# Kernel optimization log

Hardware: AMD Instinct MI355X
Metric: run time of the kernel (lower is better)

## Reference

```python
import jax, jax.numpy as jnp
import numpy as np

N_EMBED = 1024
N_HEAD = 16
HEAD_DIM = N_EMBED // N_HEAD
B, T = 64, 256
EPS = 1e-5


def _layernorm(x, w, b):
    mu = jnp.mean(x, axis=-1, keepdims=True)
    var = jnp.mean(jnp.square(x - mu), axis=-1, keepdims=True)
    return (x - mu) * jax.lax.rsqrt(var + EPS) * w + b


def setup_inputs() -> dict:
    key = jax.random.key(0)
    ks = jax.random.split(key, 8)
    s = lambda fan_in: 1.0 / np.sqrt(fan_in)
    return {
        "x": jax.random.normal(ks[0], (B, T, N_EMBED), dtype=jnp.float32),
        "ln1_w": jnp.ones((N_EMBED,), jnp.float32),
        "ln1_b": jnp.zeros((N_EMBED,), jnp.float32),
        # weights stored [in, out] (transposed vs torch Linear)
        "w_attn": jax.random.normal(ks[1], (N_EMBED, 3 * N_EMBED), jnp.float32) * s(N_EMBED),
        "b_attn": jnp.zeros((3 * N_EMBED,), jnp.float32),
        "w_proj": jax.random.normal(ks[2], (N_EMBED, N_EMBED), jnp.float32) * s(N_EMBED),
        "b_proj": jnp.zeros((N_EMBED,), jnp.float32),
        "ln2_w": jnp.ones((N_EMBED,), jnp.float32),
        "ln2_b": jnp.zeros((N_EMBED,), jnp.float32),
        "w_fc": jax.random.normal(ks[3], (N_EMBED, 4 * N_EMBED), jnp.float32) * s(N_EMBED),
        "b_fc": jnp.zeros((4 * N_EMBED,), jnp.float32),
        "w_out": jax.random.normal(ks[4], (4 * N_EMBED, N_EMBED), jnp.float32) * s(4 * N_EMBED),
        "b_out": jnp.zeros((N_EMBED,), jnp.float32),
    }


def reference(x, ln1_w, ln1_b, w_attn, b_attn, w_proj, b_proj,
              ln2_w, ln2_b, w_fc, b_fc, w_out, b_out):
    Bs, Ts, C = x.shape
    # --- attention branch (pre-norm) ---
    h = _layernorm(x, ln1_w, ln1_b)
    qkv = h @ w_attn + b_attn                      # [B,T,3C]
    q, k, v = jnp.split(qkv, 3, axis=-1)
    q = q.reshape(Bs, Ts, N_HEAD, HEAD_DIM).transpose(0, 2, 1, 3)  # [B,H,T,D]
    k = k.reshape(Bs, Ts, N_HEAD, HEAD_DIM).transpose(0, 2, 1, 3)
    v = v.reshape(Bs, Ts, N_HEAD, HEAD_DIM).transpose(0, 2, 1, 3)
    att = jnp.einsum("bhqd,bhkd->bhqk", q, k) * (1.0 / np.sqrt(HEAD_DIM))
    causal = jnp.tril(jnp.ones((Ts, Ts), dtype=bool))
    att = jnp.where(causal, att, -jnp.inf)
    att = jax.nn.softmax(att, axis=-1)
    y = jnp.einsum("bhqk,bhkd->bhqd", att, v)      # [B,H,T,D]
    y = y.transpose(0, 2, 1, 3).reshape(Bs, Ts, C)
    x = x + (y @ w_proj + b_proj)
    # --- MLP branch (pre-norm) ---
    h = _layernorm(x, ln2_w, ln2_b)
    h = jax.nn.gelu(h @ w_fc + b_fc, approximate=False)
    x = x + (h @ w_out + b_out)
    return x
```

## Files before the change

kernel.cpp:

```cpp
#include <hip/hip_runtime.h>
#include <math.h>


#define C_DIM   1024
#define NHEAD   16
#define HDIM    64
#define TSEQ    256
#define BATCH   64
#define KTILE   128

typedef __attribute__((ext_vector_type(4))) float fx4;
typedef __attribute__((ext_vector_type(8))) short sx8;

__device__ __forceinline__ ushort f2bf(float f) {
    uint x = __float_as_uint(f);
    x += 0x7fffu + ((x >> 16) & 1u);
    return (ushort)(x >> 16);
}
__device__ __forceinline__ float bf2f(ushort u) {
    return __uint_as_float(((uint)u) << 16);
}

__global__ __launch_bounds__(256)
void wconv(const float* __restrict__ W, ushort* __restrict__ Wt, int K, int N)
{
    __shared__ float T[64][65];
    const int kt = blockIdx.x << 6, nt = blockIdx.y << 6;
    const int ln = threadIdx.x & 63, g4 = threadIdx.x >> 6;
    #pragma unroll
    for (int i = 0; i < 16; ++i) {
        const int r = i * 4 + g4;
        T[r][ln] = W[(size_t)(kt + r) * N + nt + ln];
    }
    __syncthreads();
    #pragma unroll
    for (int i = 0; i < 16; ++i) {
        const int r = i * 4 + g4;
        Wt[(size_t)(nt + r) * K + kt + ln] = f2bf(T[ln][r]);
    }
}

__global__ __launch_bounds__(256)
void ln_bf16(const float* __restrict__ x, const float* __restrict__ w,
             const float* __restrict__ b, ushort* __restrict__ out)
{
    const int row = blockIdx.x;
    const int tid = threadIdx.x;
    const float4 v = reinterpret_cast<const float4*>(x + (size_t)row * C_DIM)[tid];

    float s  = v.x + v.y + v.z + v.w;
    float ss = v.x * v.x + v.y * v.y + v.z * v.z + v.w * v.w;
    #pragma unroll
    for (int off = 32; off > 0; off >>= 1) {
        s  += __shfl_down(s, off);
        ss += __shfl_down(ss, off);
    }
    __shared__ float rs[4], rss[4];
    const int wid = tid >> 6, lane = tid & 63;
    if (lane == 0) { rs[wid] = s; rss[wid] = ss; }
    __syncthreads();
    if (tid == 0) {
        const float S  = rs[0] + rs[1] + rs[2] + rs[3];
        const float SS = rss[0] + rss[1] + rss[2] + rss[3];
        const float mu  = S * (1.0f / C_DIM);
        const float var = SS * (1.0f / C_DIM) - mu * mu;
        rs[0]  = mu;
        rss[0] = rsqrtf(var + 1e-5f);
    }
    __syncthreads();
    const float mu = rs[0], rstd = rss[0];

    const float4 wv = reinterpret_cast<const float4*>(w)[tid];
    const float4 bv = reinterpret_cast<const float4*>(b)[tid];
    ushort4 o;
    o.x = f2bf((v.x - mu) * rstd * wv.x + bv.x);
    o.y = f2bf((v.y - mu) * rstd * wv.y + bv.y);
    o.z = f2bf((v.z - mu) * rstd * wv.z + bv.z);
    o.w = f2bf((v.w - mu) * rstd * wv.w + bv.w);
    reinterpret_cast<ushort4*>(out + (size_t)row * C_DIM)[tid] = o;
}

template<int EPI>
__global__ __launch_bounds__(256)
void gemm_mfma(const ushort* __restrict__ A, const ushort* __restrict__ Wt,
               const float* __restrict__ bias, const float* __restrict__ res,
               void* __restrict__ outv, int M, int N, int K)
{
    __shared__ ushort As[128 * 32];
    __shared__ ushort Bs[128 * 32];

    const int tid  = threadIdx.x;
    const int lane = tid & 63;
    const int wid  = tid >> 6;
    const int wr   = (wid >> 1) << 6;
    const int wc   = (wid & 1) << 6;
    const int bm = blockIdx.x << 7;
    const int bn = blockIdx.y << 7;

    const int srow = tid >> 2;
    const int spos = tid & 3;
    const int skg  = spos ^ ((srow >> 1) & 3);
    const size_t ga0 = (size_t)(bm + srow)      * K + skg * 8;
    const size_t ga1 = (size_t)(bm + srow + 64) * K + skg * 8;
    const size_t gb0 = (size_t)(bn + srow)      * K + skg * 8;
    const size_t gb1 = (size_t)(bn + srow + 64) * K + skg * 8;
    ushort* la0 = &As[srow * 32 + spos * 8];
    ushort* la1 = &As[(srow + 64) * 32 + spos * 8];
    ushort* lb0 = &Bs[srow * 32 + spos * 8];
    ushort* lb1 = &Bs[(srow + 64) * 32 + spos * 8];

    const int frow = lane & 15;
    const int fpos = ((lane >> 4) ^ ((frow >> 1) & 3)) * 8;
    int aoff[4], boff[4];
    #pragma unroll
    for (int i = 0; i < 4; ++i) {
        aoff[i] = (wr + i * 16 + frow) * 32 + fpos;
        boff[i] = (wc + i * 16 + frow) * 32 + fpos;
    }

    fx4 acc[4][4] = {};

    const int nk = K >> 5;
    sx8 ra0 = *(const sx8*)(A  + ga0);
    sx8 ra1 = *(const sx8*)(A  + ga1);
    sx8 rb0 = *(const sx8*)(Wt + gb0);
    sx8 rb1 = *(const sx8*)(Wt + gb1);

    for (int t = 0; t < nk; ++t) {
        __syncthreads();
        *(sx8*)la0 = ra0; *(sx8*)la1 = ra1;
        *(sx8*)lb0 = rb0; *(sx8*)lb1 = rb1;
        __syncthreads();
        if (t + 1 < nk) {
            const int ko = (t + 1) << 5;
            ra0 = *(const sx8*)(A  + ga0 + ko);
            ra1 = *(const sx8*)(A  + ga1 + ko);
            rb0 = *(const sx8*)(Wt + gb0 + ko);
            rb1 = *(const sx8*)(Wt + gb1 + ko);
        }
        sx8 af[4], bf[4];
        #pragma unroll
        for (int i = 0; i < 4; ++i) af[i] = *(const sx8*)&As[aoff[i]];
        #pragma unroll
        for (int i = 0; i < 4; ++i) bf[i] = *(const sx8*)&Bs[boff[i]];
        #pragma unroll
        for (int i = 0; i < 4; ++i)
            #pragma unroll
            for (int j = 0; j < 4; ++j)
                acc[i][j] = __builtin_amdgcn_mfma_f32_16x16x32_bf16(
                    af[i], bf[j], acc[i][j], 0, 0, 0);
    }

    const int r0 = bm + wr + (lane >> 4) * 4;
    const int c0 = bn + wc + (lane & 15);
    #pragma unroll
    for (int i = 0; i < 4; ++i) {
        #pragma unroll
        for (int r = 0; r < 4; ++r) {
            const int row = r0 + i * 16 + r;
            #pragma unroll
            for (int j = 0; j < 4; ++j) {
                const int col = c0 + j * 16;
                float v = acc[i][j][r] + bias[col];
                if (EPI == 1) {
                    v += res[(size_t)row * N + col];
                    ((float*)outv)[(size_t)row * N + col] = v;
                } else if (EPI == 2) {
                    v = 0.5f * v * (1.0f + erff(v * 0.70710678118654752f));
                    ((ushort*)outv)[(size_t)row * N + col] = f2bf(v);
                } else {
                    ((ushort*)outv)[(size_t)row * N + col] = f2bf(v);
                }
            }
        }
    }
}

__global__ __launch_bounds__(256)
void attn_kernel(const ushort* __restrict__ qkv, ushort* __restrict__ y)
{
    __shared__ float Ks[KTILE][HDIM];
    __shared__ float Vs[KTILE][HDIM];

    const int bl = blockIdx.x >> 4;
    const int h  = blockIdx.x & 15;
    const size_t base = (size_t)bl * TSEQ * 3072 + (size_t)h * HDIM;

    const int t = threadIdx.x;
    float q[HDIM];
    const ushort* qp = qkv + base + (size_t)t * 3072;
    #pragma unroll
    for (int i = 0; i < 8; ++i) {
        sx8 v8 = *(const sx8*)(qp + i * 8);
        #pragma unroll
        for (int j = 0; j < 8; ++j) q[i * 8 + j] = bf2f((ushort)v8[j]);
    }

    float acc[HDIM];
    #pragma unroll
    for (int d = 0; d < HDIM; ++d) acc[d] = 0.0f;
    float m = -INFINITY, l = 0.0f;
    const float scale = 0.125f;

    for (int ts = 0; ts < TSEQ; ts += KTILE) {
        __syncthreads();
        for (int idx = threadIdx.x; idx < KTILE * 8; idx += 256) {
            const int row = idx >> 3;
            const int c8  = (idx & 7) * 8;
            const ushort* p = qkv + base + (size_t)(ts + row) * 3072 + c8;
            sx8 kv = *(const sx8*)(p + 1024);
            sx8 vv = *(const sx8*)(p + 2048);
            #pragma unroll
            for (int j = 0; j < 8; ++j) {
                Ks[row][c8 + j] = bf2f((ushort)kv[j]);
                Vs[row][c8 + j] = bf2f((ushort)vv[j]);
            }
        }
        __syncthreads();

        const int ke = (t < ts + KTILE ? t : ts + KTILE - 1);
        for (int k = ts; k <= ke; ++k) {
            const int kr = k - ts;
            float s = 0.0f;
            #pragma unroll
            for (int d = 0; d < HDIM; ++d) s += q[d] * Ks[kr][d];
            s *= scale;
            const float mn = fmaxf(m, s);
            const float cold = __expf(m - mn);
            const float p    = __expf(s - mn);
            l = l * cold + p;
            #pragma unroll
            for (int d = 0; d < HDIM; ++d) acc[d] = acc[d] * cold + p * Vs[kr][d];
            m = mn;
        }
    }

    const float inv = 1.0f / l;
    ushort* yp = y + ((size_t)(bl * TSEQ + t)) * C_DIM + (size_t)h * HDIM;
    #pragma unroll
    for (int i = 0; i < 16; ++i) {
        ushort4 o;
        o.x = f2bf(acc[i * 4 + 0] * inv);
        o.y = f2bf(acc[i * 4 + 1] * inv);
        o.z = f2bf(acc[i * 4 + 2] * inv);
        o.w = f2bf(acc[i * 4 + 3] * inv);
        reinterpret_cast<ushort4*>(yp)[i] = o;
    }
}

extern "C" void kernel_launch(void* const* d_in, const int* in_sizes, int n_in,
                              void* d_out, int out_size, void* d_ws, size_t ws_size,
                              hipStream_t stream)
{
    const float* x      = (const float*)d_in[0];
    const float* ln1_w  = (const float*)d_in[1];
    const float* ln1_b  = (const float*)d_in[2];
    const float* w_attn = (const float*)d_in[3];
    const float* b_attn = (const float*)d_in[4];
    const float* w_proj = (const float*)d_in[5];
    const float* b_proj = (const float*)d_in[6];
    const float* ln2_w  = (const float*)d_in[7];
    const float* ln2_b  = (const float*)d_in[8];
    const float* w_fc   = (const float*)d_in[9];
    const float* b_fc   = (const float*)d_in[10];
    const float* w_out  = (const float*)d_in[11];
    const float* b_out  = (const float*)d_in[12];
    float* out = (float*)d_out;

    ushort* wbf     = (ushort*)d_ws;
    ushort* wt_attn = wbf;
    ushort* wt_proj = wbf + 3145728;
    ushort* wt_fc   = wbf + 4194304;
    ushort* wt_out  = wbf + 8388608;
    const size_t wbytes = 12582912ull * 2;

    int nchunk = 64;
    for (int cand = 1; cand <= 64; cand *= 2) {
        const size_t rows = (size_t)(BATCH / cand) * TSEQ;
        if (wbytes + rows * 10240ull <= ws_size) { nchunk = cand; break; }
    }
    const int bchunk = BATCH / nchunk;
    const int rows   = bchunk * TSEQ;

    ushort* hbuf = wbf + 12582912;
    ushort* qkvb = hbuf + (size_t)rows * 1024;
    ushort* ybuf = qkvb + (size_t)rows * 3072;
    ushort* act  = qkvb;

    wconv<<<dim3(16, 48), 256, 0, stream>>>(w_attn, wt_attn, 1024, 3072);
    wconv<<<dim3(16, 16), 256, 0, stream>>>(w_proj, wt_proj, 1024, 1024);
    wconv<<<dim3(16, 64), 256, 0, stream>>>(w_fc,   wt_fc,   1024, 4096);
    wconv<<<dim3(64, 16), 256, 0, stream>>>(w_out,  wt_out,  4096, 1024);

    for (int c = 0; c < nchunk; ++c) {
        const size_t r0 = (size_t)c * rows;
        const float* xc = x   + r0 * C_DIM;
        float*       oc = out + r0 * C_DIM;
        ln_bf16<<<rows, 256, 0, stream>>>(xc, ln1_w, ln1_b, hbuf);
        gemm_mfma<0><<<dim3(rows / 128, 3072 / 128), 256, 0, stream>>>(
            hbuf, wt_attn, b_attn, nullptr, qkvb, rows, 3072, 1024);
        attn_kernel<<<bchunk * NHEAD, 256, 0, stream>>>(qkvb, ybuf);
        gemm_mfma<1><<<dim3(rows / 128, 1024 / 128), 256, 0, stream>>>(
            ybuf, wt_proj, b_proj, xc, oc, rows, 1024, 1024);
    }

    for (int c = 0; c < nchunk; ++c) {
        const size_t r0 = (size_t)c * rows;
        float* oc = out + r0 * C_DIM;
        ln_bf16<<<rows, 256, 0, stream>>>(oc, ln2_w, ln2_b, hbuf);
        gemm_mfma<2><<<dim3(rows / 128, 4096 / 128), 256, 0, stream>>>(
            hbuf, wt_fc, b_fc, nullptr, act, rows, 4096, 1024);
        gemm_mfma<1><<<dim3(rows / 128, 1024 / 128), 256, 0, stream>>>(
            act, wt_out, b_out, oc, oc, rows, 1024, 4096);
    }
}
```

Measured before the change: 1.104 ms.

## Rewrite causal attention as MFMA flash-attention with bf16 LDS tiles

Replaces the scalar one-thread-per-query attention with a kernel where each wave handles 64 query rows. QK^T and PV use bf16 MFMA 16x16x32, and K plus transposed V are staged in LDS as bf16. Online softmax uses cross-lane shuffles, and probabilities are written to per-wave LDS before the PV multiply. Causal tiles above the diagonal are skipped. Load is unbalanced across waves, and P is rounded to bf16.

```diff
diff --git a/kernel.cpp b/kernel.cpp
--- a/kernel.cpp
+++ b/kernel.cpp
@@ -7,7 +7,6 @@
 #define HDIM    64
 #define TSEQ    256
 #define BATCH   64
-#define KTILE   128
 
 typedef __attribute__((ext_vector_type(4))) float fx4;
 typedef __attribute__((ext_vector_type(8))) short sx8;
@@ -176,76 +175,148 @@
     }
 }
 
-__global__ __launch_bounds__(256)
-void attn_kernel(const ushort* __restrict__ qkv, ushort* __restrict__ y)
-{
-    __shared__ float Ks[KTILE][HDIM];
-    __shared__ float Vs[KTILE][HDIM];
+__global__ __launch_bounds__(256, 1)
+void attn_mfma(const ushort* __restrict__ qkv, ushort* __restrict__ y)
+{
+    __shared__ ushort Ks[256 * 72];
+    __shared__ ushort Vt[64 * 264];
+    __shared__ ushort Pl[4][64 * 72];
 
     const int bl = blockIdx.x >> 4;
     const int h  = blockIdx.x & 15;
     const size_t base = (size_t)bl * TSEQ * 3072 + (size_t)h * HDIM;
 
-    const int t = threadIdx.x;
-    float q[HDIM];
-    const ushort* qp = qkv + base + (size_t)t * 3072;
-    #pragma unroll
-    for (int i = 0; i < 8; ++i) {
-        sx8 v8 = *(const sx8*)(qp + i * 8);
-        #pragma unroll
-        for (int j = 0; j < 8; ++j) q[i * 8 + j] = bf2f((ushort)v8[j]);
-    }
-
-    float acc[HDIM];
-    #pragma unroll
-    for (int d = 0; d < HDIM; ++d) acc[d] = 0.0f;
-    float m = -INFINITY, l = 0.0f;
-    const float scale = 0.125f;
-
-    for (int ts = 0; ts < TSEQ; ts += KTILE) {
-        __syncthreads();
-        for (int idx = threadIdx.x; idx < KTILE * 8; idx += 256) {
-            const int row = idx >> 3;
-            const int c8  = (idx & 7) * 8;
-            const ushort* p = qkv + base + (size_t)(ts + row) * 3072 + c8;
-            sx8 kv = *(const sx8*)(p + 1024);
-            sx8 vv = *(const sx8*)(p + 2048);
-            #pragma unroll
-            for (int j = 0; j < 8; ++j) {
-                Ks[row][c8 + j] = bf2f((ushort)kv[j]);
-                Vs[row][c8 + j] = bf2f((ushort)vv[j]);
+    const int tid  = threadIdx.x;
+    const int lane = tid & 63;
+    const int w    = tid >> 6;
+    const int c15  = lane & 15;
+    const int grp  = lane >> 4;
+
+    {
+        const int kv = tid;
+        const ushort* kp = qkv + base + (size_t)kv * 3072 + 1024;
+        const ushort* vp = qkv + base + (size_t)kv * 3072 + 2048;
+        #pragma unroll
+        for (int j = 0; j < 8; ++j) {
+            sx8 k8 = *(const sx8*)(kp + j * 8);
+            *(sx8*)&Ks[kv * 72 + j * 8] = k8;
+            sx8 v8 = *(const sx8*)(vp + j * 8);
+            #pragma unroll
+            for (int e = 0; e < 8; ++e)
+                Vt[(j * 8 + e) * 264 + kv] = (ushort)v8[e];
+        }
+    }
+
+    sx8 aq[4][2];
+    #pragma unroll
+    for (int m = 0; m < 4; ++m)
+        #pragma unroll
+        for (int kc = 0; kc < 2; ++kc) {
+            const int qr = w * 64 + m * 16 + c15;
+            aq[m][kc] = *(const sx8*)(qkv + base + (size_t)qr * 3072 + kc * 32 + grp * 8);
+        }
+
+    __syncthreads();
+
+    fx4 oacc[4][4] = {};
+    float m_s[4][4], l_s[4][4];
+    #pragma unroll
+    for (int m = 0; m < 4; ++m)
+        #pragma unroll
+        for (int r = 0; r < 4; ++r) { m_s[m][r] = -INFINITY; l_s[m][r] = 0.0f; }
+
+    for (int t = 0; t <= w; ++t) {
+        const int kt = t * 64;
+        const bool diag = (t == w);
+
+        fx4 s[4][4] = {};
+        #pragma unroll
+        for (int kc = 0; kc < 2; ++kc)
+            #pragma unroll
+            for (int n = 0; n < 4; ++n) {
+                sx8 bk = *(const sx8*)&Ks[(kt + n * 16 + c15) * 72 + kc * 32 + grp * 8];
+                #pragma unroll
+                for (int m = 0; m < 4; ++m)
+                    s[m][n] = __builtin_amdgcn_mfma_f32_16x16x32_bf16(
+                        aq[m][kc], bk, s[m][n], 0, 0, 0);
             }
-        }
-        __syncthreads();
-
-        const int ke = (t < ts + KTILE ? t : ts + KTILE - 1);
-        for (int k = ts; k <= ke; ++k) {
-            const int kr = k - ts;
-            float s = 0.0f;
-            #pragma unroll
-            for (int d = 0; d < HDIM; ++d) s += q[d] * Ks[kr][d];
-            s *= scale;
-            const float mn = fmaxf(m, s);
-            const float cold = __expf(m - mn);
-            const float p    = __expf(s - mn);
-            l = l * cold + p;
-            #pragma unroll
-            for (int d = 0; d < HDIM; ++d) acc[d] = acc[d] * cold + p * Vs[kr][d];
-            m = mn;
-        }
-    }
-
-    const float inv = 1.0f / l;
-    ushort* yp = y + ((size_t)(bl * TSEQ + t)) * C_DIM + (size_t)h * HDIM;
-    #pragma unroll
-    for (int i = 0; i < 16; ++i) {
-        ushort4 o;
-        o.x = f2bf(acc[i * 4 + 0] * inv);
-        o.y = f2bf(acc[i * 4 + 1] * inv);
-        o.z = f2bf(acc[i * 4 + 2] * inv);
-        o.w = f2bf(acc[i * 4 + 3] * inv);
-        reinterpret_cast<ushort4*>(yp)[i] = o;
-    }
+
+        #pragma unroll
+        for (int m = 0; m < 4; ++m)
+            #pragma unroll
+            for (int n = 0; n < 4; ++n)
+                #pragma unroll
+                for (int r = 0; r < 4; ++r) {
+                    float v = s[m][n][r] * 0.125f;
+                    if (diag && (n * 16 + c15) > (m * 16 + grp * 4 + r)) v = -1e30f;
+                    s[m][n][r] = v;
+                }
+
+        #pragma unroll
+        for (int m = 0; m < 4; ++m)
+            #pragma unroll
+            for (int r = 0; r < 4; ++r) {
+                float mx = fmaxf(fmaxf(s[m][0][r], s[m][1][r]),
+                                 fmaxf(s[m][2][r], s[m][3][r]));
+                #pragma unroll
+                for (int off = 1; off < 16; off <<= 1)
+                    mx = fmaxf(mx, __shfl_xor(mx, off));
+                const float mnew = fmaxf(m_s[m][r], mx);
+                const float cold = __expf(m_s[m][r] - mnew);
+                m_s[m][r] = mnew;
+                float rsum = 0.0f;
+                #pragma unroll
+                for (int n = 0; n < 4; ++n) {
+                    const float p = __expf(s[m][n][r] - mnew);
+                    s[m][n][r] = p;
+                    rsum += p;
+                }
+                #pragma unroll
+                for (int off = 1; off < 16; off <<= 1)
+                    rsum += __shfl_xor(rsum, off);
+                l_s[m][r] = l_s[m][r] * cold + rsum;
+                #pragma unroll
+                for (int dn = 0; dn < 4; ++dn)
+                    oacc[m][dn][r] *= cold;
+            }
+
+        #pragma unroll
+        for (int m = 0; m < 4; ++m)
+            #pragma unroll
+            for (int n = 0; n < 4; ++n)
+                #pragma unroll
+                for (int r = 0; r < 4; ++r)
+                    Pl[w][(m * 16 + grp * 4 + r) * 72 + n * 16 + c15] =
+                        f2bf(s[m][n][r]);
+
+        #pragma unroll
+        for (int kc = 0; kc < 2; ++kc) {
+            sx8 ap[4];
+            #pragma unroll
+            for (int m = 0; m < 4; ++m)
+                ap[m] = *(const sx8*)&Pl[w][(m * 16 + c15) * 72 + kc * 32 + grp * 8];
+            #pragma unroll
+            for (int dn = 0; dn < 4; ++dn) {
+                sx8 bv = *(const sx8*)&Vt[(dn * 16 + c15) * 264 + kt + kc * 32 + grp * 8];
+                #pragma unroll
+                for (int m = 0; m < 4; ++m)
+                    oacc[m][dn] = __builtin_amdgcn_mfma_f32_16x16x32_bf16(
+                        ap[m], bv, oacc[m][dn], 0, 0, 0);
+            }
+        }
+    }
+
+    #pragma unroll
+    for (int m = 0; m < 4; ++m)
+        #pragma unroll
+        for (int r = 0; r < 4; ++r) {
+            const float inv = 1.0f / l_s[m][r];
+            const int row = bl * TSEQ + w * 64 + m * 16 + grp * 4 + r;
+            ushort* yp = y + (size_t)row * C_DIM + h * HDIM;
+            #pragma unroll
+            for (int dn = 0; dn < 4; ++dn)
+                yp[dn * 16 + c15] = f2bf(oacc[m][dn][r] * inv);
+        }
 }
 
 extern "C" void kernel_launch(void* const* d_in, const int* in_sizes, int n_in,
@@ -299,7 +370,7 @@
         ln_bf16<<<rows, 256, 0, stream>>>(xc, ln1_w, ln1_b, hbuf);
         gemm_mfma<0><<<dim3(rows / 128, 3072 / 128), 256, 0, stream>>>(
             hbuf, wt_attn, b_attn, nullptr, qkvb, rows, 3072, 1024);
-        attn_kernel<<<bchunk * NHEAD, 256, 0, stream>>>(qkvb, ybuf);
+        attn_mfma<<<bchunk * NHEAD, 256, 0, stream>>>(qkvb, ybuf);
         gemm_mfma<1><<<dim3(rows / 128, 1024 / 128), 256, 0, stream>>>(
             ybuf, wt_proj, b_proj, xc, oc, rows, 1024, 1024);
     }
```

After: 907.5 us. 17.8% less time.
